# Performance work log

Measured on AMD Instinct MI355X. Metric: run time of the kernel, lower is better.

The kernel has to match this reference:

```python
import jax, jax.numpy as jnp
import numpy as np

B, S, T = 64, 64, 64          # batch, encoder seq len, decoder context_length
V, D, H, L = 32000, 512, 1024, 256  # vocab, embed, hidden, latent


def _gru_cell(x, h, W_ih, W_hh, b_ih, b_hh):
    # PyTorch GRUCell math. x:[B,D_in], h:[B,H]
    gi = x @ W_ih.T + b_ih            # [B,3H]
    gh = h @ W_hh.T + b_hh            # [B,3H]
    i_r, i_z, i_n = jnp.split(gi, 3, axis=-1)
    h_r, h_z, h_n = jnp.split(gh, 3, axis=-1)
    r = jax.nn.sigmoid(i_r + h_r)
    z = jax.nn.sigmoid(i_z + h_z)
    n = jnp.tanh(i_n + r * h_n)
    return (1.0 - z) * n + z * h


def setup_inputs() -> dict:
    key = jax.random.key(0)
    ks = jax.random.split(key, 16)
    s = 0.02
    inp = {
        "x": jax.random.randint(ks[0], (B, S), 0, V),
        "eps": jax.random.normal(ks[1], (B, L), dtype=jnp.float32),
        "E": jax.random.normal(ks[2], (V, D), dtype=jnp.float32) * s,
        # encoder GRU
        "W_ih_enc": jax.random.normal(ks[3], (3 * H, D), dtype=jnp.float32) * s,
        "W_hh_enc": jax.random.normal(ks[4], (3 * H, H), dtype=jnp.float32) * s,
        "b_ih_enc": jnp.zeros((3 * H,), jnp.float32),
        "b_hh_enc": jnp.zeros((3 * H,), jnp.float32),
        # latent heads
        "W_mu": jax.random.normal(ks[5], (L, H), dtype=jnp.float32) * s,
        "b_mu": jnp.zeros((L,), jnp.float32),
        "W_lv": jax.random.normal(ks[6], (L, H), dtype=jnp.float32) * s,
        "b_lv": jnp.zeros((L,), jnp.float32),
        # decoder proj_h: latent -> hidden
        "W_proj": jax.random.normal(ks[7], (H, L), dtype=jnp.float32) * s,
        "b_proj": jnp.zeros((H,), jnp.float32),
        # decoder GRU cell
        "W_ih_dec": jax.random.normal(ks[8], (3 * H, D), dtype=jnp.float32) * s,
        "W_hh_dec": jax.random.normal(ks[9], (3 * H, H), dtype=jnp.float32) * s,
        "b_ih_dec": jnp.zeros((3 * H,), jnp.float32),
        "b_hh_dec": jnp.zeros((3 * H,), jnp.float32),
        # output projection hidden -> vocab
        "W_out": jax.random.normal(ks[10], (V, H), dtype=jnp.float32) * s,
        "b_out": jnp.zeros((V,), jnp.float32),
    }
    return inp


def reference(x, eps, E, W_ih_enc, W_hh_enc, b_ih_enc, b_hh_enc,
              W_mu, b_mu, W_lv, b_lv, W_proj, b_proj,
              W_ih_dec, W_hh_dec, b_ih_dec, b_hh_dec, W_out, b_out):
    # --- encode ---
    xe = E[x]                                  # [B,S,D]
    h0 = jnp.zeros((x.shape[0], H), xe.dtype)

    def enc_step(h, xt):
        h = _gru_cell(xt, h, W_ih_enc, W_hh_enc, b_ih_enc, b_hh_enc)
        return h, None

    h_last, _ = jax.lax.scan(enc_step, h0, jnp.swapaxes(xe, 0, 1))  # scan over S
    mu = h_last @ W_mu.T + b_mu                # [B,L]
    logvar = h_last @ W_lv.T + b_lv            # [B,L]

    # --- reparametrize ---
    z = mu + eps * jnp.exp(0.5 * logvar)       # [B,L]

    h_dec0 = z @ W_proj.T + b_proj             # [B,H]
    x0 = jnp.zeros((x.shape[0], D), xe.dtype)  # step 0 input is None -> zeros

    def dec_step(carry, _):
        h, xin = carry
        h = _gru_cell(xin, h, W_ih_dec, W_hh_dec, b_ih_dec, b_hh_dec)
        logits = h @ W_out.T + b_out           # [B,V]
        nxt = jnp.argmax(logits, axis=-1)      # [B]
        return (h, E[nxt]), logits

    _, logits_seq = jax.lax.scan(dec_step, (h_dec0, x0), None, length=T)
    outputs = jnp.swapaxes(logits_seq, 0, 1)   # [B,T,V]
    return outputs, mu, logvar
```

## Files before the change

### kernel.cpp

```cpp
#include <hip/hip_runtime.h>

#define B_ 64
#define S_ 64
#define T_ 64
#define V_ 32000
#define D_ 512
#define H_ 1024
#define L_ 256

typedef _Float16 f16;
typedef __attribute__((ext_vector_type(4))) _Float16 f16x4;
typedef __attribute__((ext_vector_type(8))) _Float16 f16x8;
typedef __attribute__((ext_vector_type(16))) float f32x16;

#define INV2048 (1.0f / 2048.0f)

__device__ __forceinline__ void write_frag(f16* __restrict__ Aohi, f16* __restrict__ Aolo,
                                           int b, int j, float hv) {
  const f16 hi = (f16)hv;
  const f16 lo = (f16)((hv - (float)hi) * 2048.0f);
  const long long fo =
      (((long long)(b >> 5) * 64 + (j >> 4)) * 64 + ((b & 31) + 32 * ((j >> 3) & 1))) * 8 + (j & 7);
  Aohi[fo] = hi;
  Aolo[fo] = lo;
}

template <int K>
__global__ __launch_bounds__(256) void k_pack_wf(
    const float* __restrict__ W, f16* __restrict__ Bhi, f16* __restrict__ Blo)
{
  const int n = blockIdx.x;
  const int k = threadIdx.x * 4;
  if (k >= K) return;
  float4 w = *reinterpret_cast<const float4*>(W + (long long)n * K + k);
  float wv[4] = {w.x, w.y, w.z, w.w};
  f16x4 hi, lo;
#pragma unroll
  for (int i = 0; i < 4; ++i) {
    const f16 h = (f16)wv[i];
    hi[i] = h;
    lo[i] = (f16)((wv[i] - (float)h) * 2048.0f);
  }
  const int nt = n >> 5;
  const int lane = (n & 31) + 32 * ((k >> 3) & 1);
  const int ks = k >> 4;
  const long long off = (((long long)nt * (K / 16) + ks) * 64 + lane) * 8 + (k & 7);
  *reinterpret_cast<f16x4*>(Bhi + off) = hi;
  *reinterpret_cast<f16x4*>(Blo + off) = lo;
}

__global__ __launch_bounds__(128) void k_pack_xe(
    const int* __restrict__ x, const float* __restrict__ E,
    f16* __restrict__ XAhi, f16* __restrict__ XAlo)
{
  const int m = blockIdx.x;
  const int s = m >> 6, b = m & 63;
  const int k = threadIdx.x * 4;
  const long long tok = x[b * S_ + s];
  float4 w = *reinterpret_cast<const float4*>(E + tok * D_ + k);
  float wv[4] = {w.x, w.y, w.z, w.w};
  f16x4 hi, lo;
#pragma unroll
  for (int i = 0; i < 4; ++i) {
    const f16 h = (f16)wv[i];
    hi[i] = h;
    lo[i] = (f16)((wv[i] - (float)h) * 2048.0f);
  }
  const int mt = m >> 5;
  const int lane = (m & 31) + 32 * ((k >> 3) & 1);
  const int ks = k >> 4;
  const long long off = (((long long)mt * 32 + ks) * 64 + lane) * 8 + (k & 7);
  *reinterpret_cast<f16x4*>(XAhi + off) = hi;
  *reinterpret_cast<f16x4*>(XAlo + off) = lo;
}

__global__ __launch_bounds__(256) void k_gates_mfma(
    const f16* __restrict__ XAhi, const f16* __restrict__ XAlo,
    const f16* __restrict__ Bhi, const f16* __restrict__ Blo,
    const float* __restrict__ b_ih, float* __restrict__ Gi)
{
  __shared__ float cand[4][64][33];
  const int tid = threadIdx.x;
  const int lane = tid & 63;
  const int wv = __builtin_amdgcn_readfirstlane(tid >> 6);
  const int s = blockIdx.x / 24;
  const int ng = blockIdx.x % 24;
  const int nt = ng * 4 + wv;

  f32x16 aM0, aM1, aLa0, aLa1, aLb0, aLb1;
#pragma unroll
  for (int i = 0; i < 16; ++i) {
    aM0[i] = 0.f; aM1[i] = 0.f; aLa0[i] = 0.f; aLa1[i] = 0.f; aLb0[i] = 0.f; aLb1[i] = 0.f;
  }

  const f16x8* pB_h = reinterpret_cast<const f16x8*>(Bhi) + ((long long)nt * 32) * 64 + lane;
  const f16x8* pB_l = reinterpret_cast<const f16x8*>(Blo) + ((long long)nt * 32) * 64 + lane;
  const f16x8* pA_h = reinterpret_cast<const f16x8*>(XAhi) + ((long long)s * 64) * 64 + lane;
  const f16x8* pA_l = reinterpret_cast<const f16x8*>(XAlo) + ((long long)s * 64) * 64 + lane;

#pragma unroll 4
  for (int ks = 0; ks < 32; ++ks) {
    const int o = ks * 64;
    f16x8 bh = pB_h[o];
    f16x8 bl = pB_l[o];
    f16x8 a0 = pA_h[o];
    f16x8 a1 = pA_h[o + 32 * 64];
    f16x8 l0 = pA_l[o];
    f16x8 l1 = pA_l[o + 32 * 64];
    aM0 = __builtin_amdgcn_mfma_f32_32x32x16_f16(a0, bh, aM0, 0, 0, 0);
    aM1 = __builtin_amdgcn_mfma_f32_32x32x16_f16(a1, bh, aM1, 0, 0, 0);
    aLa0 = __builtin_amdgcn_mfma_f32_32x32x16_f16(a0, bl, aLa0, 0, 0, 0);
    aLa1 = __builtin_amdgcn_mfma_f32_32x32x16_f16(a1, bl, aLa1, 0, 0, 0);
    aLb0 = __builtin_amdgcn_mfma_f32_32x32x16_f16(l0, bh, aLb0, 0, 0, 0);
    aLb1 = __builtin_amdgcn_mfma_f32_32x32x16_f16(l1, bh, aLb1, 0, 0, 0);
  }

  {
    const int l = lane & 31;
    const int rbase = 4 * (lane >> 5);
#pragma unroll
    for (int reg = 0; reg < 16; ++reg) {
      const int row = (reg & 3) + 8 * (reg >> 2) + rbase;
      cand[wv][row][l] = aM0[reg] + (aLa0[reg] + aLb0[reg]) * INV2048;
      cand[wv][row + 32][l] = aM1[reg] + (aLa1[reg] + aLb1[reg]) * INV2048;
    }
  }
  __syncthreads();
  const int bn0 = ng * 128;
#pragma unroll
  for (int i = 0; i < 8; ++i) {
    const int idx = i * 256 + tid;
    const int b4 = (idx & 15) * 4;
    const int nl = idx >> 4;
    const float bi = b_ih[bn0 + nl];
    float4 o;
    o.x = cand[nl >> 5][b4 + 0][nl & 31] + bi;
    o.y = cand[nl >> 5][b4 + 1][nl & 31] + bi;
    o.z = cand[nl >> 5][b4 + 2][nl & 31] + bi;
    o.w = cand[nl >> 5][b4 + 3][nl & 31] + bi;
    *reinterpret_cast<float4*>(&Gi[((long long)s * (3 * H_) + bn0 + nl) * 64 + b4]) = o;
  }
}

__global__ __launch_bounds__(256) void k_hh_mfma(
    const f16* __restrict__ Ahi, const f16* __restrict__ Alo,
    const f16* __restrict__ Bhi, const f16* __restrict__ Blo,
    float* __restrict__ preH)
{
  __shared__ float cand[4][64][33];
  const int tid = threadIdx.x;
  const int lane = tid & 63;
  const int wv = __builtin_amdgcn_readfirstlane(tid >> 6);
  const int nt = blockIdx.x;

  f32x16 aM0, aM1, aLa0, aLa1, aLb0, aLb1;
#pragma unroll
  for (int i = 0; i < 16; ++i) {
    aM0[i] = 0.f; aM1[i] = 0.f; aLa0[i] = 0.f; aLa1[i] = 0.f; aLb0[i] = 0.f; aLb1[i] = 0.f;
  }

  const f16x8* pB_h = reinterpret_cast<const f16x8*>(Bhi) + ((long long)nt * 64 + wv * 16) * 64 + lane;
  const f16x8* pB_l = reinterpret_cast<const f16x8*>(Blo) + ((long long)nt * 64 + wv * 16) * 64 + lane;
  const f16x8* pA_h = reinterpret_cast<const f16x8*>(Ahi) + (long long)(wv * 16) * 64 + lane;
  const f16x8* pA_l = reinterpret_cast<const f16x8*>(Alo) + (long long)(wv * 16) * 64 + lane;

#pragma unroll 4
  for (int q = 0; q < 16; ++q) {
    const int o = q * 64;
    f16x8 bh = pB_h[o];
    f16x8 bl = pB_l[o];
    f16x8 a0 = pA_h[o];
    f16x8 a1 = pA_h[o + 4096];
    f16x8 l0 = pA_l[o];
    f16x8 l1 = pA_l[o + 4096];
    aM0 = __builtin_amdgcn_mfma_f32_32x32x16_f16(a0, bh, aM0, 0, 0, 0);
    aM1 = __builtin_amdgcn_mfma_f32_32x32x16_f16(a1, bh, aM1, 0, 0, 0);
    aLa0 = __builtin_amdgcn_mfma_f32_32x32x16_f16(a0, bl, aLa0, 0, 0, 0);
    aLa1 = __builtin_amdgcn_mfma_f32_32x32x16_f16(a1, bl, aLa1, 0, 0, 0);
    aLb0 = __builtin_amdgcn_mfma_f32_32x32x16_f16(l0, bh, aLb0, 0, 0, 0);
    aLb1 = __builtin_amdgcn_mfma_f32_32x32x16_f16(l1, bh, aLb1, 0, 0, 0);
  }

  {
    const int l = lane & 31;
    const int rbase = 4 * (lane >> 5);
#pragma unroll
    for (int reg = 0; reg < 16; ++reg) {
      const int row = (reg & 3) + 8 * (reg >> 2) + rbase;
      cand[wv][row][l] = aM0[reg] + (aLa0[reg] + aLb0[reg]) * INV2048;
      cand[wv][row + 32][l] = aM1[reg] + (aLa1[reg] + aLb1[reg]) * INV2048;
    }
  }
  __syncthreads();
#pragma unroll
  for (int i = 0; i < 8; ++i) {
    const int idx = i * 256 + tid;
    const int b = idx & 63;
    const int l = idx >> 6;
    const float v = cand[0][b][l] + cand[1][b][l] + cand[2][b][l] + cand[3][b][l];
    preH[((long long)nt * 32 + l) * 64 + b] = v;
  }
}

__global__ __launch_bounds__(256) void k_apply_enc(
    const float* __restrict__ preH, const float* __restrict__ Gi_t,
    const float* __restrict__ b_hh,
    const float* __restrict__ hT_in, float* __restrict__ hT_out,
    f16* __restrict__ Aohi, f16* __restrict__ Aolo)
{
  const int idx = blockIdx.x * 256 + threadIdx.x;
  const int b = idx & 63;
  const int j = idx >> 6;
  const float gr = preH[(long long)j * 64 + b] + Gi_t[(long long)j * 64 + b] + b_hh[j];
  const float gz = preH[(long long)(H_ + j) * 64 + b] + Gi_t[(long long)(H_ + j) * 64 + b] + b_hh[H_ + j];
  const float gin = Gi_t[(long long)(2 * H_ + j) * 64 + b];
  const float ghn = preH[(long long)(2 * H_ + j) * 64 + b] + b_hh[2 * H_ + j];
  const float r = 1.f / (1.f + expf(-gr));
  const float z = 1.f / (1.f + expf(-gz));
  const float n = tanhf(fmaf(r, ghn, gin));
  const float hp = hT_in[(long long)j * 64 + b];
  const float hv = (1.f - z) * n + z * hp;
  hT_out[(long long)j * 64 + b] = hv;
  write_frag(Aohi, Aolo, b, j, hv);
}

template <int XMODE>
__global__ __launch_bounds__(1024) void k_dec_apply(
    const float* __restrict__ E, const unsigned long long* __restrict__ bp,
    const float* __restrict__ W_ih,
    const float* __restrict__ b_ih, const float* __restrict__ b_hh,
    const float* __restrict__ preH, const float* __restrict__ hT_in,
    float* __restrict__ hT_out, f16* __restrict__ Aohi, f16* __restrict__ Aolo)
{
  __shared__ float4 a_lds[64 * 64];
  __shared__ float red[12 * 3 * 64];
  __shared__ int toks[64];
  const int tid = threadIdx.x;
  const int lane = tid & 63;
  const int wv = __builtin_amdgcn_readfirstlane(tid >> 6);
  const int jj = wv & 3;
  const int ks = wv >> 2;
  const int j = blockIdx.x * 4 + jj;
  const int kf16 = tid & 63;
  const int msub = tid >> 6;

  float accR = 0.f, accZ = 0.f, accIN = 0.f;

  if constexpr (XMODE == 2) {
#pragma unroll
    for (int rr = 0; rr < 4; ++rr) {
      const int r = wv + rr * 16;
      unsigned long long kk = 0ull;
#pragma unroll
      for (int i = 0; i < 8; ++i) {
        const unsigned long long q = bp[(long long)r * 512 + lane + i * 64];
        if (q > kk) kk = q;
      }
#pragma unroll
      for (int m = 1; m < 64; m <<= 1) {
        const unsigned long long q = __shfl_xor(kk, m, 64);
        if (q > kk) kk = q;
      }
      if (lane == 0) toks[r] = (int)(0xFFFFFFFFu - (unsigned)(kk & 0xFFFFFFFFull));
    }
    __syncthreads();

    const float* wr = W_ih + (long long)j * D_;
    const float* wz = W_ih + (long long)(j + H_) * D_;
    const float* wn = W_ih + (long long)(j + 2 * H_) * D_;
    for (int c = 0; c < 2; ++c) {
      __syncthreads();
#pragma unroll
      for (int p = 0; p < 4; ++p) {
        const int m = p * 16 + msub;
        const long long tok = toks[m];
        float4 v = *reinterpret_cast<const float4*>(E + tok * D_ + c * 256 + kf16 * 4);
        a_lds[m * 64 + (kf16 ^ (m & 7))] = v;
      }
      __syncthreads();
#pragma unroll 4
      for (int q = 0; q < 16; ++q) {
        const int kf = ks * 16 + q;
        float4 a = a_lds[lane * 64 + (kf ^ (lane & 7))];
        float4 w0 = *reinterpret_cast<const float4*>(wr + c * 256 + kf * 4);
        float4 w1 = *reinterpret_cast<const float4*>(wz + c * 256 + kf * 4);
        float4 w2 = *reinterpret_cast<const float4*>(wn + c * 256 + kf * 4);
        accR = fmaf(w0.x, a.x, accR); accR = fmaf(w0.y, a.y, accR);
        accR = fmaf(w0.z, a.z, accR); accR = fmaf(w0.w, a.w, accR);
        accZ = fmaf(w1.x, a.x, accZ); accZ = fmaf(w1.y, a.y, accZ);
        accZ = fmaf(w1.z, a.z, accZ); accZ = fmaf(w1.w, a.w, accZ);
        accIN = fmaf(w2.x, a.x, accIN); accIN = fmaf(w2.y, a.y, accIN);
        accIN = fmaf(w2.z, a.z, accIN); accIN = fmaf(w2.w, a.w, accIN);
      }
    }
  }

  if (ks > 0) {
    float* rp = red + (((ks - 1) * 4 + jj) * 3) * 64 + lane;
    rp[0] = accR; rp[64] = accZ; rp[128] = accIN;
  }
  __syncthreads();
  if (ks == 0) {
#pragma unroll
    for (int t2 = 0; t2 < 3; ++t2) {
      const float* rp = red + ((t2 * 4 + jj) * 3) * 64 + lane;
      accR += rp[0]; accZ += rp[64]; accIN += rp[128];
    }
    const float gr = accR + preH[(long long)j * 64 + lane] + b_ih[j] + b_hh[j];
    const float gz = accZ + preH[(long long)(H_ + j) * 64 + lane] + b_ih[H_ + j] + b_hh[H_ + j];
    const float gin = accIN + b_ih[2 * H_ + j];
    const float ghn = preH[(long long)(2 * H_ + j) * 64 + lane] + b_hh[2 * H_ + j];
    const float r = 1.f / (1.f + expf(-gr));
    const float z = 1.f / (1.f + expf(-gz));
    const float n = tanhf(fmaf(r, ghn, gin));
    const float hp = hT_in[(long long)j * 64 + lane];
    const float hv = (1.f - z) * n + z * hp;
    hT_out[(long long)j * 64 + lane] = hv;
    write_frag(Aohi, Aolo, lane, j, hv);
  }
}

__global__ __launch_bounds__(256) void k_logits_hh(
    const f16* __restrict__ Ahi, const f16* __restrict__ Alo,
    const f16* __restrict__ WOhi, const f16* __restrict__ WOlo,
    const f16* __restrict__ WHhi, const f16* __restrict__ WHlo,
    const float* __restrict__ b_out, float* __restrict__ out,
    unsigned long long* __restrict__ bestPart, float* __restrict__ preH, int t)
{
  __shared__ float cand[4][64][33];
  __shared__ unsigned long long wbest[4][64];
  const int tid = threadIdx.x;
  const int lane = tid & 63;
  const int wv = __builtin_amdgcn_readfirstlane(tid >> 6);

  if (blockIdx.x >= 500) {
    const int hhb = blockIdx.x - 500;
    const int nt = hhb * 4 + wv;
    f32x16 aM0, aM1, aLa0, aLa1, aLb0, aLb1;
#pragma unroll
    for (int i = 0; i < 16; ++i) {
      aM0[i] = 0.f; aM1[i] = 0.f; aLa0[i] = 0.f; aLa1[i] = 0.f; aLb0[i] = 0.f; aLb1[i] = 0.f;
    }
    const f16x8* pB_h = reinterpret_cast<const f16x8*>(WHhi) + ((long long)nt * 64) * 64 + lane;
    const f16x8* pB_l = reinterpret_cast<const f16x8*>(WHlo) + ((long long)nt * 64) * 64 + lane;
    const f16x8* pA_h = reinterpret_cast<const f16x8*>(Ahi) + lane;
    const f16x8* pA_l = reinterpret_cast<const f16x8*>(Alo) + lane;
#pragma unroll 4
    for (int ksi = 0; ksi < 64; ++ksi) {
      const int o = ksi * 64;
      f16x8 bh = pB_h[o];
      f16x8 bl = pB_l[o];
      f16x8 a0 = pA_h[o];
      f16x8 a1 = pA_h[o + 4096];
      f16x8 l0 = pA_l[o];
      f16x8 l1 = pA_l[o + 4096];
      aM0 = __builtin_amdgcn_mfma_f32_32x32x16_f16(a0, bh, aM0, 0, 0, 0);
      aM1 = __builtin_amdgcn_mfma_f32_32x32x16_f16(a1, bh, aM1, 0, 0, 0);
      aLa0 = __builtin_amdgcn_mfma_f32_32x32x16_f16(a0, bl, aLa0, 0, 0, 0);
      aLa1 = __builtin_amdgcn_mfma_f32_32x32x16_f16(a1, bl, aLa1, 0, 0, 0);
      aLb0 = __builtin_amdgcn_mfma_f32_32x32x16_f16(l0, bh, aLb0, 0, 0, 0);
      aLb1 = __builtin_amdgcn_mfma_f32_32x32x16_f16(l1, bh, aLb1, 0, 0, 0);
    }
    {
      const int l = lane & 31;
      const int rbase = 4 * (lane >> 5);
#pragma unroll
      for (int reg = 0; reg < 16; ++reg) {
        const int row = (reg & 3) + 8 * (reg >> 2) + rbase;
        cand[wv][row][l] = aM0[reg] + (aLa0[reg] + aLb0[reg]) * INV2048;
        cand[wv][row + 32][l] = aM1[reg] + (aLa1[reg] + aLb1[reg]) * INV2048;
      }
    }
    __syncthreads();
#pragma unroll
    for (int i = 0; i < 8; ++i) {
      const int idx = i * 256 + tid;
      const int b4 = (idx & 15) * 4;
      const int nl = idx >> 4;
      float4 o;
      o.x = cand[nl >> 5][b4 + 0][nl & 31];
      o.y = cand[nl >> 5][b4 + 1][nl & 31];
      o.z = cand[nl >> 5][b4 + 2][nl & 31];
      o.w = cand[nl >> 5][b4 + 3][nl & 31];
      *reinterpret_cast<float4*>(&preH[((long long)hhb * 128 + nl) * 64 + b4]) = o;
    }
    return;
  }

  const int p = wv >> 1;
  const int kh = wv & 1;
  const int nt = blockIdx.x * 2 + p;

  f32x16 accM0, accM1, accL0, accL1;
#pragma unroll
  for (int i = 0; i < 16; ++i) { accM0[i] = 0.f; accM1[i] = 0.f; accL0[i] = 0.f; accL1[i] = 0.f; }

  const int kb = kh * 32 * 64;
  const f16x8* pAh0 = reinterpret_cast<const f16x8*>(Ahi) + kb + lane;
  const f16x8* pAh1 = reinterpret_cast<const f16x8*>(Ahi) + 4096 + kb + lane;
  const f16x8* pAl0 = reinterpret_cast<const f16x8*>(Alo) + kb + lane;
  const f16x8* pAl1 = reinterpret_cast<const f16x8*>(Alo) + 4096 + kb + lane;
  const f16x8* pBh = reinterpret_cast<const f16x8*>(WOhi) + (long long)nt * 4096 + kb + lane;
  const f16x8* pBl = reinterpret_cast<const f16x8*>(WOlo) + (long long)nt * 4096 + kb + lane;

#pragma unroll 4
  for (int ksi = 0; ksi < 32; ++ksi) {
    const int o = ksi * 64;
    f16x8 bh = pBh[o];
    f16x8 bl = pBl[o];
    f16x8 ah0 = pAh0[o];
    f16x8 ah1 = pAh1[o];
    f16x8 al0 = pAl0[o];
    f16x8 al1 = pAl1[o];
    accM0 = __builtin_amdgcn_mfma_f32_32x32x16_f16(ah0, bh, accM0, 0, 0, 0);
    accM1 = __builtin_amdgcn_mfma_f32_32x32x16_f16(ah1, bh, accM1, 0, 0, 0);
    accL0 = __builtin_amdgcn_mfma_f32_32x32x16_f16(ah0, bl, accL0, 0, 0, 0);
    accL1 = __builtin_amdgcn_mfma_f32_32x32x16_f16(ah1, bl, accL1, 0, 0, 0);
    accL0 = __builtin_amdgcn_mfma_f32_32x32x16_f16(al0, bh, accL0, 0, 0, 0);
    accL1 = __builtin_amdgcn_mfma_f32_32x32x16_f16(al1, bh, accL1, 0, 0, 0);
  }

  const int l31 = lane & 31;
  const int rbase = 4 * (lane >> 5);

  if (kh == 1) {
#pragma unroll
    for (int reg = 0; reg < 16; ++reg) {
      const int row0 = (reg & 3) + 8 * (reg >> 2) + rbase;
      cand[2 + p][row0][l31] = accM0[reg] + accL0[reg] * INV2048;
      cand[2 + p][row0 + 32][l31] = accM1[reg] + accL1[reg] * INV2048;
    }
  }
  __syncthreads();
  if (kh == 0) {
    const int nn = nt * 32 + l31;
    const float bo = b_out[nn];
#pragma unroll
    for (int reg = 0; reg < 16; ++reg) {
      const int row0 = (reg & 3) + 8 * (reg >> 2) + rbase;
      const float v0 = accM0[reg] + accL0[reg] * INV2048 + cand[2 + p][row0][l31] + bo;
      __builtin_nontemporal_store(v0, &out[(long long)row0 * (T_ * (long long)V_) + (long long)t * V_ + nn]);
      const int row1 = row0 + 32;
      const float v1 = accM1[reg] + accL1[reg] * INV2048 + cand[2 + p][row1][l31] + bo;
      __builtin_nontemporal_store(v1, &out[(long long)row1 * (T_ * (long long)V_) + (long long)t * V_ + nn]);
      cand[2 + p][row0][l31] = v0;
      cand[2 + p][row1][l31] = v1;
    }
  }
  __syncthreads();
  {
    const int w = tid >> 6;
    const int s = w & 1;
    const int r = tid & 63;
    const int nb = (blockIdx.x * 2 + s) * 32;
    unsigned long long kk = 0ull;
#pragma unroll
    for (int l0 = 0; l0 < 32; ++l0) {
      const int l = (l0 + r) & 31;
      const float v = cand[2 + s][r][l];
      unsigned u = __float_as_uint(v);
      u = (u & 0x80000000u) ? ~u : (u | 0x80000000u);
      const unsigned long long key = ((unsigned long long)u << 32) |
          (unsigned long long)(0xFFFFFFFFu - (unsigned)(nb + l));
      if (key > kk) kk = key;
    }
    wbest[w][r] = kk;
  }
  __syncthreads();
  if (tid < 64) {
    unsigned long long kk = wbest[0][tid];
#pragma unroll
    for (int w = 1; w < 4; ++w) { const unsigned long long q = wbest[w][tid]; if (q > kk) kk = q; }
    bestPart[(long long)tid * 512 + blockIdx.x] = kk;
  }
}

__global__ __launch_bounds__(256) void k_mu_lv_z(
    const float* __restrict__ hT, const float* __restrict__ W_mu, const float* __restrict__ b_mu,
    const float* __restrict__ W_lv, const float* __restrict__ b_lv,
    const float* __restrict__ eps, float* __restrict__ out_mu, float* __restrict__ out_lv,
    float* __restrict__ zT)
{
  const int lane = threadIdx.x & 63;
  const int wv = __builtin_amdgcn_readfirstlane(threadIdx.x >> 6);
  const int l = blockIdx.x * 4 + wv;
  const float* wm = W_mu + (long long)l * H_;
  const float* wl = W_lv + (long long)l * H_;
  float am = 0.f, av = 0.f;
#pragma unroll 8
  for (int k = 0; k < H_; ++k) {
    const float h = hT[k * 64 + lane];
    am = fmaf(wm[k], h, am);
    av = fmaf(wl[k], h, av);
  }
  const float mu = am + b_mu[l];
  const float lv = av + b_lv[l];
  out_mu[lane * L_ + l] = mu;
  out_lv[lane * L_ + l] = lv;
  zT[l * 64 + lane] = fmaf(eps[lane * L_ + l], expf(0.5f * lv), mu);
}

__global__ __launch_bounds__(256) void k_proj(
    const float* __restrict__ zT, const float* __restrict__ W_proj,
    const float* __restrict__ b_proj, float* __restrict__ hT0,
    f16* __restrict__ Aohi, f16* __restrict__ Aolo)
{
  const int lane = threadIdx.x & 63;
  const int wv = __builtin_amdgcn_readfirstlane(threadIdx.x >> 6);
  const int j = blockIdx.x * 4 + wv;
  const float* wr = W_proj + (long long)j * L_;
  float acc = 0.f;
#pragma unroll 8
  for (int k = 0; k < L_; ++k) acc = fmaf(wr[k], zT[k * 64 + lane], acc);
  const float hv = acc + b_proj[j];
  hT0[(long long)j * 64 + lane] = hv;
  write_frag(Aohi, Aolo, lane, j, hv);
}

extern "C" void kernel_launch(void* const* d_in, const int* in_sizes, int n_in,
                              void* d_out, int out_size, void* d_ws, size_t ws_size,
                              hipStream_t stream) {
  (void)in_sizes; (void)n_in; (void)out_size;
  const int*   x        = (const int*)d_in[0];
  const float* eps      = (const float*)d_in[1];
  const float* E        = (const float*)d_in[2];
  const float* W_ih_enc = (const float*)d_in[3];
  const float* W_hh_enc = (const float*)d_in[4];
  const float* b_ih_enc = (const float*)d_in[5];
  const float* b_hh_enc = (const float*)d_in[6];
  const float* W_mu     = (const float*)d_in[7];
  const float* b_mu     = (const float*)d_in[8];
  const float* W_lv     = (const float*)d_in[9];
  const float* b_lv     = (const float*)d_in[10];
  const float* W_proj   = (const float*)d_in[11];
  const float* b_proj   = (const float*)d_in[12];
  const float* W_ih_dec = (const float*)d_in[13];
  const float* W_hh_dec = (const float*)d_in[14];
  const float* b_ih_dec = (const float*)d_in[15];
  const float* b_hh_dec = (const float*)d_in[16];
  const float* W_out    = (const float*)d_in[17];
  const float* b_out    = (const float*)d_in[18];

  float* out = (float*)d_out;
  const long long OFF_MU = (long long)B_ * T_ * V_;
  const long long OFF_LV = OFF_MU + (long long)B_ * L_;

  float* ws = (float*)d_ws;
  float* hA   = ws + 0;
  float* dA   = ws + 65536;
  float* zT   = ws + 131072;
  unsigned long long* bestPart = (unsigned long long*)(ws + 147456);
  float* preH = ws + 212992;
  f16* frAhi  = (f16*)(ws + 409600);
  f16* frAlo  = (f16*)(ws + 442368);
  f16* WHEhi  = (f16*)(ws + 475136);
  f16* WHElo  = (f16*)(ws + 2048000);
  f16* WHDhi  = (f16*)(ws + 3620864);
  f16* WHDlo  = (f16*)(ws + 5193728);
  f16* WIEhi  = (f16*)(ws + 6766592);
  f16* WIElo  = (f16*)(ws + 7553024);
  f16* XAhi   = (f16*)(ws + 8339456);
  f16* XAlo   = (f16*)(ws + 9388032);
  float* Gi   = ws + 10436608;
  f16* WOhi   = (f16*)(ws + 8339456);
  f16* WOlo   = (f16*)(ws + 24723456);
  const size_t WS_NEED = (size_t)41107456 * 4;
  if (ws_size < WS_NEED) return;

  hipMemsetAsync(hA, 0, (size_t)H_ * B_ * sizeof(float), stream);
  hipMemsetAsync(frAhi, 0, (size_t)2 * 65536 * sizeof(f16), stream);
  hipMemsetAsync(bestPart, 0, (size_t)64 * 512 * 8, stream);

  k_pack_wf<1024><<<3 * H_, 256, 0, stream>>>(W_hh_enc, WHEhi, WHElo);
  k_pack_wf<1024><<<3 * H_, 256, 0, stream>>>(W_hh_dec, WHDhi, WHDlo);
  k_pack_wf<512><<<3 * H_, 128, 0, stream>>>(W_ih_enc, WIEhi, WIElo);
  k_pack_xe<<<S_ * B_, 128, 0, stream>>>(x, E, XAhi, XAlo);

  k_gates_mfma<<<64 * 24, 256, 0, stream>>>(XAhi, XAlo, WIEhi, WIElo, b_ih_enc, Gi);

  for (int t = 0; t < S_; ++t) {
    k_hh_mfma<<<96, 256, 0, stream>>>(frAhi, frAlo, WHEhi, WHElo, preH);
    k_apply_enc<<<256, 256, 0, stream>>>(preH, Gi + (long long)t * 3 * H_ * B_,
                                         b_hh_enc, hA, hA, frAhi, frAlo);
  }

  k_mu_lv_z<<<64, 256, 0, stream>>>(hA, W_mu, b_mu, W_lv, b_lv, eps,
                                    out + OFF_MU, out + OFF_LV, zT);
  k_proj<<<256, 256, 0, stream>>>(zT, W_proj, b_proj, dA, frAhi, frAlo);

  k_pack_wf<1024><<<V_, 256, 0, stream>>>(W_out, WOhi, WOlo);

  k_hh_mfma<<<96, 256, 0, stream>>>(frAhi, frAlo, WHDhi, WHDlo, preH);

  for (int t = 0; t < T_; ++t) {
    if (t == 0) {
      k_dec_apply<0><<<256, 1024, 0, stream>>>(
          E, nullptr, W_ih_dec, b_ih_dec, b_hh_dec, preH, dA, dA, frAhi, frAlo);
    } else {
      k_dec_apply<2><<<256, 1024, 0, stream>>>(
          E, bestPart, W_ih_dec, b_ih_dec, b_hh_dec, preH, dA, dA, frAhi, frAlo);
    }
    k_logits_hh<<<524, 256, 0, stream>>>(frAhi, frAlo, WOhi, WOlo, WHDhi, WHDlo,
                                         b_out, out, bestPart, preH, t);
  }
}
```

Measured before the change: 6.257 ms.

## Fuse GRU hidden matmul with gate apply and move decoder input gates to MFMA

Each encoder step now runs a single fused kernel that computes the recurrent matmul for all three gates of a 32-column slice and applies the GRU update in place. This replaces the separate hh-matmul and apply kernels and ping-pongs the f16 hi/lo fragment buffers between steps. The decoder input-gate matvec moves from scalar FP32 FMAs to split-f16 MFMA fed by on-the-fly embedding conversion, and the logits kernel is re-split into 1000 single-tile blocks with a four-way K split. The two low-order correction MFMAs now share one accumulator. The fused step kernels launch only 32 blocks, which may underuse the GPU, and the packed decoder weights need extra workspace.

Result: slower. 7.534 ms (+20.4%).

```diff
diff --git a/kernel.cpp b/kernel.cpp
--- a/kernel.cpp
+++ b/kernel.cpp
@@ -25,6 +25,16 @@
   Aolo[fo] = lo;
 }
 
+__device__ __forceinline__ void cvt8(const float4& v0, const float4& v1, f16x8& hi, f16x8& lo) {
+  float vv[8] = {v0.x, v0.y, v0.z, v0.w, v1.x, v1.y, v1.z, v1.w};
+#pragma unroll
+  for (int e = 0; e < 8; ++e) {
+    const f16 h = (f16)vv[e];
+    hi[e] = h;
+    lo[e] = (f16)((vv[e] - (float)h) * 2048.0f);
+  }
+}
+
 template <int K>
 __global__ __launch_bounds__(256) void k_pack_wf(
     const float* __restrict__ W, f16* __restrict__ Bhi, f16* __restrict__ Blo)
@@ -87,11 +97,9 @@
   const int ng = blockIdx.x % 24;
   const int nt = ng * 4 + wv;
 
-  f32x16 aM0, aM1, aLa0, aLa1, aLb0, aLb1;
-#pragma unroll
-  for (int i = 0; i < 16; ++i) {
-    aM0[i] = 0.f; aM1[i] = 0.f; aLa0[i] = 0.f; aLa1[i] = 0.f; aLb0[i] = 0.f; aLb1[i] = 0.f;
-  }
+  f32x16 aM0, aM1, aL0, aL1;
+#pragma unroll
+  for (int i = 0; i < 16; ++i) { aM0[i] = 0.f; aM1[i] = 0.f; aL0[i] = 0.f; aL1[i] = 0.f; }
 
   const f16x8* pB_h = reinterpret_cast<const f16x8*>(Bhi) + ((long long)nt * 32) * 64 + lane;
   const f16x8* pB_l = reinterpret_cast<const f16x8*>(Blo) + ((long long)nt * 32) * 64 + lane;
@@ -109,10 +117,10 @@
     f16x8 l1 = pA_l[o + 32 * 64];
     aM0 = __builtin_amdgcn_mfma_f32_32x32x16_f16(a0, bh, aM0, 0, 0, 0);
     aM1 = __builtin_amdgcn_mfma_f32_32x32x16_f16(a1, bh, aM1, 0, 0, 0);
-    aLa0 = __builtin_amdgcn_mfma_f32_32x32x16_f16(a0, bl, aLa0, 0, 0, 0);
-    aLa1 = __builtin_amdgcn_mfma_f32_32x32x16_f16(a1, bl, aLa1, 0, 0, 0);
-    aLb0 = __builtin_amdgcn_mfma_f32_32x32x16_f16(l0, bh, aLb0, 0, 0, 0);
-    aLb1 = __builtin_amdgcn_mfma_f32_32x32x16_f16(l1, bh, aLb1, 0, 0, 0);
+    aL0 = __builtin_amdgcn_mfma_f32_32x32x16_f16(a0, bl, aL0, 0, 0, 0);
+    aL0 = __builtin_amdgcn_mfma_f32_32x32x16_f16(l0, bh, aL0, 0, 0, 0);
+    aL1 = __builtin_amdgcn_mfma_f32_32x32x16_f16(a1, bl, aL1, 0, 0, 0);
+    aL1 = __builtin_amdgcn_mfma_f32_32x32x16_f16(l1, bh, aL1, 0, 0, 0);
   }
 
   {
@@ -121,8 +129,8 @@
 #pragma unroll
     for (int reg = 0; reg < 16; ++reg) {
       const int row = (reg & 3) + 8 * (reg >> 2) + rbase;
-      cand[wv][row][l] = aM0[reg] + (aLa0[reg] + aLb0[reg]) * INV2048;
-      cand[wv][row + 32][l] = aM1[reg] + (aLa1[reg] + aLb1[reg]) * INV2048;
+      cand[wv][row][l] = aM0[reg] + aL0[reg] * INV2048;
+      cand[wv][row + 32][l] = aM1[reg] + aL1[reg] * INV2048;
     }
   }
   __syncthreads();
@@ -153,11 +161,9 @@
   const int wv = __builtin_amdgcn_readfirstlane(tid >> 6);
   const int nt = blockIdx.x;
 
-  f32x16 aM0, aM1, aLa0, aLa1, aLb0, aLb1;
-#pragma unroll
-  for (int i = 0; i < 16; ++i) {
-    aM0[i] = 0.f; aM1[i] = 0.f; aLa0[i] = 0.f; aLa1[i] = 0.f; aLb0[i] = 0.f; aLb1[i] = 0.f;
-  }
+  f32x16 aM0, aM1, aL0, aL1;
+#pragma unroll
+  for (int i = 0; i < 16; ++i) { aM0[i] = 0.f; aM1[i] = 0.f; aL0[i] = 0.f; aL1[i] = 0.f; }
 
   const f16x8* pB_h = reinterpret_cast<const f16x8*>(Bhi) + ((long long)nt * 64 + wv * 16) * 64 + lane;
   const f16x8* pB_l = reinterpret_cast<const f16x8*>(Blo) + ((long long)nt * 64 + wv * 16) * 64 + lane;
@@ -175,10 +181,10 @@
     f16x8 l1 = pA_l[o + 4096];
     aM0 = __builtin_amdgcn_mfma_f32_32x32x16_f16(a0, bh, aM0, 0, 0, 0);
     aM1 = __builtin_amdgcn_mfma_f32_32x32x16_f16(a1, bh, aM1, 0, 0, 0);
-    aLa0 = __builtin_amdgcn_mfma_f32_32x32x16_f16(a0, bl, aLa0, 0, 0, 0);
-    aLa1 = __builtin_amdgcn_mfma_f32_32x32x16_f16(a1, bl, aLa1, 0, 0, 0);
-    aLb0 = __builtin_amdgcn_mfma_f32_32x32x16_f16(l0, bh, aLb0, 0, 0, 0);
-    aLb1 = __builtin_amdgcn_mfma_f32_32x32x16_f16(l1, bh, aLb1, 0, 0, 0);
+    aL0 = __builtin_amdgcn_mfma_f32_32x32x16_f16(a0, bl, aL0, 0, 0, 0);
+    aL0 = __builtin_amdgcn_mfma_f32_32x32x16_f16(l0, bh, aL0, 0, 0, 0);
+    aL1 = __builtin_amdgcn_mfma_f32_32x32x16_f16(a1, bl, aL1, 0, 0, 0);
+    aL1 = __builtin_amdgcn_mfma_f32_32x32x16_f16(l1, bh, aL1, 0, 0, 0);
   }
 
   {
@@ -187,8 +193,8 @@
 #pragma unroll
     for (int reg = 0; reg < 16; ++reg) {
       const int row = (reg & 3) + 8 * (reg >> 2) + rbase;
-      cand[wv][row][l] = aM0[reg] + (aLa0[reg] + aLb0[reg]) * INV2048;
-      cand[wv][row + 32][l] = aM1[reg] + (aLa1[reg] + aLb1[reg]) * INV2048;
+      cand[wv][row][l] = aM0[reg] + aL0[reg] * INV2048;
+      cand[wv][row + 32][l] = aM1[reg] + aL1[reg] * INV2048;
     }
   }
   __syncthreads();
@@ -202,58 +208,113 @@
   }
 }
 
-__global__ __launch_bounds__(256) void k_apply_enc(
-    const float* __restrict__ preH, const float* __restrict__ Gi_t,
-    const float* __restrict__ b_hh,
-    const float* __restrict__ hT_in, float* __restrict__ hT_out,
-    f16* __restrict__ Aohi, f16* __restrict__ Aolo)
-{
-  const int idx = blockIdx.x * 256 + threadIdx.x;
-  const int b = idx & 63;
-  const int j = idx >> 6;
-  const float gr = preH[(long long)j * 64 + b] + Gi_t[(long long)j * 64 + b] + b_hh[j];
-  const float gz = preH[(long long)(H_ + j) * 64 + b] + Gi_t[(long long)(H_ + j) * 64 + b] + b_hh[H_ + j];
-  const float gin = Gi_t[(long long)(2 * H_ + j) * 64 + b];
-  const float ghn = preH[(long long)(2 * H_ + j) * 64 + b] + b_hh[2 * H_ + j];
-  const float r = 1.f / (1.f + expf(-gr));
-  const float z = 1.f / (1.f + expf(-gz));
-  const float n = tanhf(fmaf(r, ghn, gin));
-  const float hp = hT_in[(long long)j * 64 + b];
-  const float hv = (1.f - z) * n + z * hp;
-  hT_out[(long long)j * 64 + b] = hv;
-  write_frag(Aohi, Aolo, b, j, hv);
+__global__ __launch_bounds__(256, 2) void k_enc_step(
+    const float* __restrict__ Gi_t,
+    const f16* __restrict__ WHhi, const f16* __restrict__ WHlo,
+    const float* __restrict__ b_hh, float* __restrict__ hT,
+    const f16* __restrict__ fin_hi, const f16* __restrict__ fin_lo,
+    f16* __restrict__ fout_hi, f16* __restrict__ fout_lo)
+{
+  __shared__ float cand[4][64][33];
+  const int tid = threadIdx.x;
+  const int lane = tid & 63;
+  const int wv = __builtin_amdgcn_readfirstlane(tid >> 6);
+  const int c = blockIdx.x;
+
+  float pr[3][8];
+#pragma unroll
+  for (int g = 0; g < 3; ++g) {
+    f32x16 aM0, aM1, aL0, aL1;
+#pragma unroll
+    for (int i = 0; i < 16; ++i) { aM0[i] = 0.f; aM1[i] = 0.f; aL0[i] = 0.f; aL1[i] = 0.f; }
+    const f16x8* pBh = reinterpret_cast<const f16x8*>(WHhi) + ((long long)(g * 32 + c) * 64 + wv * 16) * 64 + lane;
+    const f16x8* pBl = reinterpret_cast<const f16x8*>(WHlo) + ((long long)(g * 32 + c) * 64 + wv * 16) * 64 + lane;
+    const f16x8* pAh = reinterpret_cast<const f16x8*>(fin_hi) + (long long)(wv * 16) * 64 + lane;
+    const f16x8* pAl = reinterpret_cast<const f16x8*>(fin_lo) + (long long)(wv * 16) * 64 + lane;
+#pragma unroll 4
+    for (int q = 0; q < 16; ++q) {
+      const int o = q * 64;
+      f16x8 bh = pBh[o];
+      f16x8 bl = pBl[o];
+      f16x8 a0 = pAh[o];
+      f16x8 a1 = pAh[o + 4096];
+      f16x8 l0 = pAl[o];
+      f16x8 l1 = pAl[o + 4096];
+      aM0 = __builtin_amdgcn_mfma_f32_32x32x16_f16(a0, bh, aM0, 0, 0, 0);
+      aM1 = __builtin_amdgcn_mfma_f32_32x32x16_f16(a1, bh, aM1, 0, 0, 0);
+      aL0 = __builtin_amdgcn_mfma_f32_32x32x16_f16(a0, bl, aL0, 0, 0, 0);
+      aL0 = __builtin_amdgcn_mfma_f32_32x32x16_f16(l0, bh, aL0, 0, 0, 0);
+      aL1 = __builtin_amdgcn_mfma_f32_32x32x16_f16(a1, bl, aL1, 0, 0, 0);
+      aL1 = __builtin_amdgcn_mfma_f32_32x32x16_f16(l1, bh, aL1, 0, 0, 0);
+    }
+    __syncthreads();
+    {
+      const int l = lane & 31;
+      const int rbase = 4 * (lane >> 5);
+#pragma unroll
+      for (int reg = 0; reg < 16; ++reg) {
+        const int row = (reg & 3) + 8 * (reg >> 2) + rbase;
+        cand[wv][row][l] = aM0[reg] + aL0[reg] * INV2048;
+        cand[wv][row + 32][l] = aM1[reg] + aL1[reg] * INV2048;
+      }
+    }
+    __syncthreads();
+#pragma unroll
+    for (int i = 0; i < 8; ++i) {
+      const int idx = i * 256 + tid;
+      const int b = idx & 63;
+      const int l2 = idx >> 6;
+      pr[g][i] = cand[0][b][l2] + cand[1][b][l2] + cand[2][b][l2] + cand[3][b][l2];
+    }
+  }
+
+#pragma unroll
+  for (int i = 0; i < 8; ++i) {
+    const int idx = i * 256 + tid;
+    const int b = idx & 63;
+    const int j = c * 32 + (idx >> 6);
+    const float gr = pr[0][i] + Gi_t[(long long)j * 64 + b] + b_hh[j];
+    const float gz = pr[1][i] + Gi_t[(long long)(H_ + j) * 64 + b] + b_hh[H_ + j];
+    const float gin = Gi_t[(long long)(2 * H_ + j) * 64 + b];
+    const float ghn = pr[2][i] + b_hh[2 * H_ + j];
+    const float r = 1.f / (1.f + expf(-gr));
+    const float z = 1.f / (1.f + expf(-gz));
+    const float n = tanhf(fmaf(r, ghn, gin));
+    const float hp = hT[(long long)j * 64 + b];
+    const float hv = (1.f - z) * n + z * hp;
+    hT[(long long)j * 64 + b] = hv;
+    write_frag(fout_hi, fout_lo, b, j, hv);
+  }
 }
 
 template <int XMODE>
-__global__ __launch_bounds__(1024) void k_dec_apply(
+__global__ __launch_bounds__(256, 2) void k_dec_step(
     const float* __restrict__ E, const unsigned long long* __restrict__ bp,
-    const float* __restrict__ W_ih,
+    const f16* __restrict__ WIhi, const f16* __restrict__ WIlo,
     const float* __restrict__ b_ih, const float* __restrict__ b_hh,
-    const float* __restrict__ preH, const float* __restrict__ hT_in,
-    float* __restrict__ hT_out, f16* __restrict__ Aohi, f16* __restrict__ Aolo)
-{
-  __shared__ float4 a_lds[64 * 64];
-  __shared__ float red[12 * 3 * 64];
+    const float* __restrict__ preH, float* __restrict__ hT,
+    f16* __restrict__ fout_hi, f16* __restrict__ fout_lo)
+{
+  __shared__ float cand[4][64][33];
   __shared__ int toks[64];
   const int tid = threadIdx.x;
   const int lane = tid & 63;
   const int wv = __builtin_amdgcn_readfirstlane(tid >> 6);
-  const int jj = wv & 3;
-  const int ks = wv >> 2;
-  const int j = blockIdx.x * 4 + jj;
-  const int kf16 = tid & 63;
-  const int msub = tid >> 6;
-
-  float accR = 0.f, accZ = 0.f, accIN = 0.f;
+  const int c = blockIdx.x;
+
+  float pr[3][8];
+#pragma unroll
+  for (int g = 0; g < 3; ++g)
+#pragma unroll
+    for (int i = 0; i < 8; ++i) pr[g][i] = 0.f;
 
   if constexpr (XMODE == 2) {
-#pragma unroll
-    for (int rr = 0; rr < 4; ++rr) {
-      const int r = wv + rr * 16;
+    for (int rr = 0; rr < 16; ++rr) {
+      const int r = wv * 16 + rr;
       unsigned long long kk = 0ull;
 #pragma unroll
-      for (int i = 0; i < 8; ++i) {
-        const unsigned long long q = bp[(long long)r * 512 + lane + i * 64];
+      for (int s2 = 0; s2 < 16; ++s2) {
+        const unsigned long long q = bp[(long long)r * 1024 + lane + s2 * 64];
         if (q > kk) kk = q;
       }
 #pragma unroll
@@ -265,62 +326,77 @@
     }
     __syncthreads();
 
-    const float* wr = W_ih + (long long)j * D_;
-    const float* wz = W_ih + (long long)(j + H_) * D_;
-    const float* wn = W_ih + (long long)(j + 2 * H_) * D_;
-    for (int c = 0; c < 2; ++c) {
-      __syncthreads();
-#pragma unroll
-      for (int p = 0; p < 4; ++p) {
-        const int m = p * 16 + msub;
-        const long long tok = toks[m];
-        float4 v = *reinterpret_cast<const float4*>(E + tok * D_ + c * 256 + kf16 * 4);
-        a_lds[m * 64 + (kf16 ^ (m & 7))] = v;
+    const long long eb0 = (long long)toks[lane & 31] * D_ + (lane >> 5) * 8;
+    const long long eb1 = (long long)toks[32 + (lane & 31)] * D_ + (lane >> 5) * 8;
+
+#pragma unroll
+    for (int g = 0; g < 3; ++g) {
+      f32x16 aM0, aM1, aL0, aL1;
+#pragma unroll
+      for (int i = 0; i < 16; ++i) { aM0[i] = 0.f; aM1[i] = 0.f; aL0[i] = 0.f; aL1[i] = 0.f; }
+      const f16x8* pBh = reinterpret_cast<const f16x8*>(WIhi) + ((long long)(g * 32 + c) * 32 + wv * 8) * 64 + lane;
+      const f16x8* pBl = reinterpret_cast<const f16x8*>(WIlo) + ((long long)(g * 32 + c) * 32 + wv * 8) * 64 + lane;
+#pragma unroll 2
+      for (int q = 0; q < 8; ++q) {
+        const int k = (wv * 8 + q) * 16;
+        float4 v0 = *reinterpret_cast<const float4*>(E + eb0 + k);
+        float4 v1 = *reinterpret_cast<const float4*>(E + eb0 + k + 4);
+        float4 u0 = *reinterpret_cast<const float4*>(E + eb1 + k);
+        float4 u1 = *reinterpret_cast<const float4*>(E + eb1 + k + 4);
+        f16x8 a0, l0, a1, l1;
+        cvt8(v0, v1, a0, l0);
+        cvt8(u0, u1, a1, l1);
+        f16x8 bh = pBh[q * 64];
+        f16x8 bl = pBl[q * 64];
+        aM0 = __builtin_amdgcn_mfma_f32_32x32x16_f16(a0, bh, aM0, 0, 0, 0);
+        aM1 = __builtin_amdgcn_mfma_f32_32x32x16_f16(a1, bh, aM1, 0, 0, 0);
+        aL0 = __builtin_amdgcn_mfma_f32_32x32x16_f16(a0, bl, aL0, 0, 0, 0);
+        aL0 = __builtin_amdgcn_mfma_f32_32x32x16_f16(l0, bh, aL0, 0, 0, 0);
+        aL1 = __builtin_amdgcn_mfma_f32_32x32x16_f16(a1, bl, aL1, 0, 0, 0);
+        aL1 = __builtin_amdgcn_mfma_f32_32x32x16_f16(l1, bh, aL1, 0, 0, 0);
       }
       __syncthreads();
-#pragma unroll 4
-      for (int q = 0; q < 16; ++q) {
-        const int kf = ks * 16 + q;
-        float4 a = a_lds[lane * 64 + (kf ^ (lane & 7))];
-        float4 w0 = *reinterpret_cast<const float4*>(wr + c * 256 + kf * 4);
-        float4 w1 = *reinterpret_cast<const float4*>(wz + c * 256 + kf * 4);
-        float4 w2 = *reinterpret_cast<const float4*>(wn + c * 256 + kf * 4);
-        accR = fmaf(w0.x, a.x, accR); accR = fmaf(w0.y, a.y, accR);
-        accR = fmaf(w0.z, a.z, accR); accR = fmaf(w0.w, a.w, accR);
-        accZ = fmaf(w1.x, a.x, accZ); accZ = fmaf(w1.y, a.y, accZ);
-        accZ = fmaf(w1.z, a.z, accZ); accZ = fmaf(w1.w, a.w, accZ);
-        accIN = fmaf(w2.x, a.x, accIN); accIN = fmaf(w2.y, a.y, accIN);
-        accIN = fmaf(w2.z, a.z, accIN); accIN = fmaf(w2.w, a.w, accIN);
+      {
+        const int l = lane & 31;
+        const int rbase = 4 * (lane >> 5);
+#pragma unroll
+        for (int reg = 0; reg < 16; ++reg) {
+          const int row = (reg & 3) + 8 * (reg >> 2) + rbase;
+          cand[wv][row][l] = aM0[reg] + aL0[reg] * INV2048;
+          cand[wv][row + 32][l] = aM1[reg] + aL1[reg] * INV2048;
+        }
       }
-    }
-  }
-
-  if (ks > 0) {
-    float* rp = red + (((ks - 1) * 4 + jj) * 3) * 64 + lane;
-    rp[0] = accR; rp[64] = accZ; rp[128] = accIN;
-  }
-  __syncthreads();
-  if (ks == 0) {
-#pragma unroll
-    for (int t2 = 0; t2 < 3; ++t2) {
-      const float* rp = red + ((t2 * 4 + jj) * 3) * 64 + lane;
-      accR += rp[0]; accZ += rp[64]; accIN += rp[128];
-    }
-    const float gr = accR + preH[(long long)j * 64 + lane] + b_ih[j] + b_hh[j];
-    const float gz = accZ + preH[(long long)(H_ + j) * 64 + lane] + b_ih[H_ + j] + b_hh[H_ + j];
-    const float gin = accIN + b_ih[2 * H_ + j];
-    const float ghn = preH[(long long)(2 * H_ + j) * 64 + lane] + b_hh[2 * H_ + j];
+      __syncthreads();
+#pragma unroll
+      for (int i = 0; i < 8; ++i) {
+        const int idx = i * 256 + tid;
+        const int b = idx & 63;
+        const int l2 = idx >> 6;
+        pr[g][i] = cand[0][b][l2] + cand[1][b][l2] + cand[2][b][l2] + cand[3][b][l2];
+      }
+    }
+  }
+
+#pragma unroll
+  for (int i = 0; i < 8; ++i) {
+    const int idx = i * 256 + tid;
+    const int b = idx & 63;
+    const int j = c * 32 + (idx >> 6);
+    const float gr = pr[0][i] + preH[(long long)j * 64 + b] + b_ih[j] + b_hh[j];
+    const float gz = pr[1][i] + preH[(long long)(H_ + j) * 64 + b] + b_ih[H_ + j] + b_hh[H_ + j];
+    const float gin = pr[2][i] + b_ih[2 * H_ + j];
+    const float ghn = preH[(long long)(2 * H_ + j) * 64 + b] + b_hh[2 * H_ + j];
     const float r = 1.f / (1.f + expf(-gr));
     const float z = 1.f / (1.f + expf(-gz));
     const float n = tanhf(fmaf(r, ghn, gin));
-    const float hp = hT_in[(long long)j * 64 + lane];
+    const float hp = hT[(long long)j * 64 + b];
     const float hv = (1.f - z) * n + z * hp;
-    hT_out[(long long)j * 64 + lane] = hv;
-    write_frag(Aohi, Aolo, lane, j, hv);
-  }
-}
-
-__global__ __launch_bounds__(256) void k_logits_hh(
+    hT[(long long)j * 64 + b] = hv;
+    write_frag(fout_hi, fout_lo, b, j, hv);
+  }
+}
+
+__global__ __launch_bounds__(256, 4) void k_logits_hh(
     const f16* __restrict__ Ahi, const f16* __restrict__ Alo,
     const f16* __restrict__ WOhi, const f16* __restrict__ WOlo,
     const f16* __restrict__ WHhi, const f16* __restrict__ WHlo,
@@ -333,14 +409,12 @@
   const int lane = tid & 63;
   const int wv = __builtin_amdgcn_readfirstlane(tid >> 6);
 
-  if (blockIdx.x >= 500) {
-    const int hhb = blockIdx.x - 500;
+  if (blockIdx.x >= 1000) {
+    const int hhb = blockIdx.x - 1000;
     const int nt = hhb * 4 + wv;
-    f32x16 aM0, aM1, aLa0, aLa1, aLb0, aLb1;
-#pragma unroll
-    for (int i = 0; i < 16; ++i) {
-      aM0[i] = 0.f; aM1[i] = 0.f; aLa0[i] = 0.f; aLa1[i] = 0.f; aLb0[i] = 0.f; aLb1[i] = 0.f;
-    }
+    f32x16 aM0, aM1, aL0, aL1;
+#pragma unroll
+    for (int i = 0; i < 16; ++i) { aM0[i] = 0.f; aM1[i] = 0.f; aL0[i] = 0.f; aL1[i] = 0.f; }
     const f16x8* pB_h = reinterpret_cast<const f16x8*>(WHhi) + ((long long)nt * 64) * 64 + lane;
     const f16x8* pB_l = reinterpret_cast<const f16x8*>(WHlo) + ((long long)nt * 64) * 64 + lane;
     const f16x8* pA_h = reinterpret_cast<const f16x8*>(Ahi) + lane;
@@ -356,10 +430,10 @@
       f16x8 l1 = pA_l[o + 4096];
       aM0 = __builtin_amdgcn_mfma_f32_32x32x16_f16(a0, bh, aM0, 0, 0, 0);
       aM1 = __builtin_amdgcn_mfma_f32_32x32x16_f16(a1, bh, aM1, 0, 0, 0);
-      aLa0 = __builtin_amdgcn_mfma_f32_32x32x16_f16(a0, bl, aLa0, 0, 0, 0);
-      aLa1 = __builtin_amdgcn_mfma_f32_32x32x16_f16(a1, bl, aLa1, 0, 0, 0);
-      aLb0 = __builtin_amdgcn_mfma_f32_32x32x16_f16(l0, bh, aLb0, 0, 0, 0);
-      aLb1 = __builtin_amdgcn_mfma_f32_32x32x16_f16(l1, bh, aLb1, 0, 0, 0);
+      aL0 = __builtin_amdgcn_mfma_f32_32x32x16_f16(a0, bl, aL0, 0, 0, 0);
+      aL0 = __builtin_amdgcn_mfma_f32_32x32x16_f16(l0, bh, aL0, 0, 0, 0);
+      aL1 = __builtin_amdgcn_mfma_f32_32x32x16_f16(a1, bl, aL1, 0, 0, 0);
+      aL1 = __builtin_amdgcn_mfma_f32_32x32x16_f16(l1, bh, aL1, 0, 0, 0);
     }
     {
       const int l = lane & 31;
@@ -367,8 +441,8 @@
 #pragma unroll
       for (int reg = 0; reg < 16; ++reg) {
         const int row = (reg & 3) + 8 * (reg >> 2) + rbase;
-        cand[wv][row][l] = aM0[reg] + (aLa0[reg] + aLb0[reg]) * INV2048;
-        cand[wv][row + 32][l] = aM1[reg] + (aLa1[reg] + aLb1[reg]) * INV2048;
+        cand[wv][row][l] = aM0[reg] + aL0[reg] * INV2048;
+        cand[wv][row + 32][l] = aM1[reg] + aL1[reg] * INV2048;
       }
     }
     __syncthreads();
@@ -387,15 +461,12 @@
     return;
   }
 
-  const int p = wv >> 1;
-  const int kh = wv & 1;
-  const int nt = blockIdx.x * 2 + p;
-
+  const int nt = blockIdx.x;
   f32x16 accM0, accM1, accL0, accL1;
 #pragma unroll
   for (int i = 0; i < 16; ++i) { accM0[i] = 0.f; accM1[i] = 0.f; accL0[i] = 0.f; accL1[i] = 0.f; }
 
-  const int kb = kh * 32 * 64;
+  const int kb = wv * 16 * 64;
   const f16x8* pAh0 = reinterpret_cast<const f16x8*>(Ahi) + kb + lane;
   const f16x8* pAh1 = reinterpret_cast<const f16x8*>(Ahi) + 4096 + kb + lane;
   const f16x8* pAl0 = reinterpret_cast<const f16x8*>(Alo) + kb + lane;
@@ -404,7 +475,7 @@
   const f16x8* pBl = reinterpret_cast<const f16x8*>(WOlo) + (long long)nt * 4096 + kb + lane;
 
 #pragma unroll 4
-  for (int ksi = 0; ksi < 32; ++ksi) {
+  for (int ksi = 0; ksi < 16; ++ksi) {
     const int o = ksi * 64;
     f16x8 bh = pBh[o];
     f16x8 bl = pBl[o];
@@ -415,63 +486,58 @@
     accM0 = __builtin_amdgcn_mfma_f32_32x32x16_f16(ah0, bh, accM0, 0, 0, 0);
     accM1 = __builtin_amdgcn_mfma_f32_32x32x16_f16(ah1, bh, accM1, 0, 0, 0);
     accL0 = __builtin_amdgcn_mfma_f32_32x32x16_f16(ah0, bl, accL0, 0, 0, 0);
+    accL0 = __builtin_amdgcn_mfma_f32_32x32x16_f16(al0, bh, accL0, 0, 0, 0);
     accL1 = __builtin_amdgcn_mfma_f32_32x32x16_f16(ah1, bl, accL1, 0, 0, 0);
-    accL0 = __builtin_amdgcn_mfma_f32_32x32x16_f16(al0, bh, accL0, 0, 0, 0);
     accL1 = __builtin_amdgcn_mfma_f32_32x32x16_f16(al1, bh, accL1, 0, 0, 0);
   }
 
-  const int l31 = lane & 31;
-  const int rbase = 4 * (lane >> 5);
-
-  if (kh == 1) {
+  {
+    const int l31 = lane & 31;
+    const int rbase = 4 * (lane >> 5);
 #pragma unroll
     for (int reg = 0; reg < 16; ++reg) {
-      const int row0 = (reg & 3) + 8 * (reg >> 2) + rbase;
-      cand[2 + p][row0][l31] = accM0[reg] + accL0[reg] * INV2048;
-      cand[2 + p][row0 + 32][l31] = accM1[reg] + accL1[reg] * INV2048;
+      const int row = (reg & 3) + 8 * (reg >> 2) + rbase;
+      cand[wv][row][l31] = accM0[reg] + accL0[reg] * INV2048;
+      cand[wv][row + 32][l31] = accM1[reg] + accL1[reg] * INV2048;
     }
   }
   __syncthreads();
-  if (kh == 0) {
-    const int nn = nt * 32 + l31;
-    const float bo = b_out[nn];
-#pragma unroll
-    for (int reg = 0; reg < 16; ++reg) {
-      const int row0 = (reg & 3) + 8 * (reg >> 2) + rbase;
-      const float v0 = accM0[reg] + accL0[reg] * INV2048 + cand[2 + p][row0][l31] + bo;
-      __builtin_nontemporal_store(v0, &out[(long long)row0 * (T_ * (long long)V_) + (long long)t * V_ + nn]);
-      const int row1 = row0 + 32;
-      const float v1 = accM1[reg] + accL1[reg] * INV2048 + cand[2 + p][row1][l31] + bo;
-      __builtin_nontemporal_store(v1, &out[(long long)row1 * (T_ * (long long)V_) + (long long)t * V_ + nn]);
-      cand[2 + p][row0][l31] = v0;
-      cand[2 + p][row1][l31] = v1;
-    }
+
+#pragma unroll
+  for (int i = 0; i < 8; ++i) {
+    const int idx = i * 256 + tid;
+    const int col = idx & 31;
+    const int row = idx >> 5;
+    const int nn = nt * 32 + col;
+    const float v = cand[0][row][col] + cand[1][row][col] + cand[2][row][col] +
+                    cand[3][row][col] + b_out[nn];
+    __builtin_nontemporal_store(v, &out[(long long)row * (T_ * (long long)V_) + (long long)t * V_ + nn]);
+    cand[0][row][col] = v;
   }
   __syncthreads();
+
   {
-    const int w = tid >> 6;
-    const int s = w & 1;
     const int r = tid & 63;
-    const int nb = (blockIdx.x * 2 + s) * 32;
+    const int q = tid >> 6;
     unsigned long long kk = 0ull;
 #pragma unroll
-    for (int l0 = 0; l0 < 32; ++l0) {
-      const int l = (l0 + r) & 31;
-      const float v = cand[2 + s][r][l];
+    for (int cc = 0; cc < 8; ++cc) {
+      const int col = q * 8 + cc;
+      const float v = cand[0][r][col];
       unsigned u = __float_as_uint(v);
       u = (u & 0x80000000u) ? ~u : (u | 0x80000000u);
       const unsigned long long key = ((unsigned long long)u << 32) |
-          (unsigned long long)(0xFFFFFFFFu - (unsigned)(nb + l));
+          (unsigned long long)(0xFFFFFFFFu - (unsigned)(nt * 32 + col));
       if (key > kk) kk = key;
     }
-    wbest[w][r] = kk;
+    wbest[q][r] = kk;
   }
   __syncthreads();
   if (tid < 64) {
     unsigned long long kk = wbest[0][tid];
 #pragma unroll
     for (int w = 1; w < 4; ++w) { const unsigned long long q = wbest[w][tid]; if (q > kk) kk = q; }
-    bestPart[(long long)tid * 512 + blockIdx.x] = kk;
+    bestPart[(long long)tid * 1024 + blockIdx.x] = kk;
   }
 }
 
@@ -550,38 +616,46 @@
   float* dA   = ws + 65536;
   float* zT   = ws + 131072;
   unsigned long long* bestPart = (unsigned long long*)(ws + 147456);
-  float* preH = ws + 212992;
-  f16* frAhi  = (f16*)(ws + 409600);
-  f16* frAlo  = (f16*)(ws + 442368);
-  f16* WHEhi  = (f16*)(ws + 475136);
-  f16* WHElo  = (f16*)(ws + 2048000);
-  f16* WHDhi  = (f16*)(ws + 3620864);
-  f16* WHDlo  = (f16*)(ws + 5193728);
-  f16* WIEhi  = (f16*)(ws + 6766592);
-  f16* WIElo  = (f16*)(ws + 7553024);
-  f16* XAhi   = (f16*)(ws + 8339456);
-  f16* XAlo   = (f16*)(ws + 9388032);
-  float* Gi   = ws + 10436608;
-  f16* WOhi   = (f16*)(ws + 8339456);
-  f16* WOlo   = (f16*)(ws + 24723456);
-  const size_t WS_NEED = (size_t)41107456 * 4;
+  float* preH = ws + 278528;
+  f16* frAhi  = (f16*)(ws + 475136);
+  f16* frAlo  = (f16*)(ws + 507904);
+  f16* frBhi  = (f16*)(ws + 540672);
+  f16* frBlo  = (f16*)(ws + 573440);
+  f16* WHEhi  = (f16*)(ws + 606208);
+  f16* WHElo  = (f16*)(ws + 2179072);
+  f16* WHDhi  = (f16*)(ws + 3751936);
+  f16* WHDlo  = (f16*)(ws + 5324800);
+  f16* WIEhi  = (f16*)(ws + 6897664);
+  f16* WIElo  = (f16*)(ws + 7684096);
+  f16* WIDhi  = (f16*)(ws + 8470528);
+  f16* WIDlo  = (f16*)(ws + 9256960);
+  f16* XAhi   = (f16*)(ws + 10043392);
+  f16* XAlo   = (f16*)(ws + 11091968);
+  float* Gi   = ws + 12140544;
+  f16* WOhi   = (f16*)(ws + 10043392);
+  f16* WOlo   = (f16*)(ws + 26427392);
+  const size_t WS_NEED = (size_t)42811392 * 4;
   if (ws_size < WS_NEED) return;
 
   hipMemsetAsync(hA, 0, (size_t)H_ * B_ * sizeof(float), stream);
   hipMemsetAsync(frAhi, 0, (size_t)2 * 65536 * sizeof(f16), stream);
-  hipMemsetAsync(bestPart, 0, (size_t)64 * 512 * 8, stream);
+  hipMemsetAsync(bestPart, 0, (size_t)64 * 1024 * 8, stream);
 
   k_pack_wf<1024><<<3 * H_, 256, 0, stream>>>(W_hh_enc, WHEhi, WHElo);
   k_pack_wf<1024><<<3 * H_, 256, 0, stream>>>(W_hh_dec, WHDhi, WHDlo);
   k_pack_wf<512><<<3 * H_, 128, 0, stream>>>(W_ih_enc, WIEhi, WIElo);
+  k_pack_wf<512><<<3 * H_, 128, 0, stream>>>(W_ih_dec, WIDhi, WIDlo);
   k_pack_xe<<<S_ * B_, 128, 0, stream>>>(x, E, XAhi, XAlo);
 
   k_gates_mfma<<<64 * 24, 256, 0, stream>>>(XAhi, XAlo, WIEhi, WIElo, b_ih_enc, Gi);
 
   for (int t = 0; t < S_; ++t) {
-    k_hh_mfma<<<96, 256, 0, stream>>>(frAhi, frAlo, WHEhi, WHElo, preH);
-    k_apply_enc<<<256, 256, 0, stream>>>(preH, Gi + (long long)t * 3 * H_ * B_,
-                                         b_hh_enc, hA, hA, frAhi, frAlo);
+    const f16* fih = (t & 1) ? frBhi : frAhi;
+    const f16* fil = (t & 1) ? frBlo : frAlo;
+    f16* foh = (t & 1) ? frAhi : frBhi;
+    f16* fol = (t & 1) ? frAlo : frBlo;
+    k_enc_step<<<32, 256, 0, stream>>>(Gi + (long long)t * 3 * H_ * B_,
+                                       WHEhi, WHElo, b_hh_enc, hA, fih, fil, foh, fol);
   }
 
   k_mu_lv_z<<<64, 256, 0, stream>>>(hA, W_mu, b_mu, W_lv, b_lv, eps,
@@ -594,13 +668,13 @@
 
   for (int t = 0; t < T_; ++t) {
     if (t == 0) {
-      k_dec_apply<0><<<256, 1024, 0, stream>>>(
-          E, nullptr, W_ih_dec, b_ih_dec, b_hh_dec, preH, dA, dA, frAhi, frAlo);
+      k_dec_step<0><<<32, 256, 0, stream>>>(
+          E, nullptr, WIDhi, WIDlo, b_ih_dec, b_hh_dec, preH, dA, frAhi, frAlo);
     } else {
-      k_dec_apply<2><<<256, 1024, 0, stream>>>(
-          E, bestPart, W_ih_dec, b_ih_dec, b_hh_dec, preH, dA, dA, frAhi, frAlo);
-    }
-    k_logits_hh<<<524, 256, 0, stream>>>(frAhi, frAlo, WOhi, WOlo, WHDhi, WHDlo,
-                                         b_out, out, bestPart, preH, t);
-  }
-}
+      k_dec_step<2><<<32, 256, 0, stream>>>(
+          E, bestPart, WIDhi, WIDlo, b_ih_dec, b_hh_dec, preH, dA, frAhi, frAlo);
+    }
+    k_logits_hh<<<1024, 256, 0, stream>>>(frAhi, frAlo, WOhi, WOlo, WHDhi, WHDlo,
+                                          b_out, out, bestPart, preH, t);
+  }
+}
```
